# Optimization experiments

Measured on AMD Instinct MI355X. Metric: run time of the kernel, lower is better.

The kernel has to match this reference:

```python
import jax, jax.numpy as jnp
import numpy as np

K = 32          # init k
E = 0.003       # EMA rate e


def setup_inputs() -> dict:
    key = jax.random.key(0)
    k1, _ = jax.random.split(key)
    features = jax.random.normal(k1, (512, 6, 8192), dtype=jnp.float32)
    threshold = jnp.zeros((1,), dtype=jnp.float32)
    return {"features": features, "threshold": threshold}


def reference(features, threshold):
    batch_size, n_layers, d_features = features.shape
    batch_k = K * batch_size * n_layers
    flat = features.reshape(-1)                      # [B*L*D]
    topk_vals, topk_idxs = jax.lax.top_k(flat, batch_k)
    topk_vals = jax.nn.relu(topk_vals)
    out = jnp.zeros_like(flat).at[topk_idxs].set(topk_vals)
    out = out.reshape(batch_size, n_layers, d_features)
    min_k = jax.lax.stop_gradient(jnp.min(topk_vals))
    new_threshold = (1.0 - E) * threshold + E * min_k
    return out, new_threshold
```

## Files before the change

kernel.cpp:

```cpp
#include <hip/hip_runtime.h>
#include <stdint.h>

#define K_TOTAL   98304u
#define EMA_RATE  0.003f

#define SBINS      16384
#define SBIN_SHIFT 18
#define SAMPLE_VEC 131072
#define STARGET    8192u
#define P2_BINS    4096
#define P2_SHIFT   12
#define LCAP       1024
#define CAP2       65536u
#define EQCAP      256

#define MP_BLOCKS  3072
#define MP_UNROLL  8

__device__ __forceinline__ unsigned f2key(float x) {
    unsigned u = __float_as_uint(x);
    return (u & 0x80000000u) ? ~u : (u | 0x80000000u);
}
__device__ __forceinline__ float key2f(unsigned key) {
    unsigned u = (key & 0x80000000u) ? (key & 0x7FFFFFFFu) : ~key;
    return __uint_as_float(u);
}

__global__ __launch_bounds__(256) void sample_hist_kernel(
        const float4* __restrict__ in, unsigned* __restrict__ shist) {
    __shared__ unsigned h[SBINS];
    for (int i = threadIdx.x; i < SBINS; i += 256) h[i] = 0;
    __syncthreads();
    unsigned tid = blockIdx.x * 256 + threadIdx.x;
    unsigned nth = gridDim.x * 256;
    float4 v[4];
    #pragma unroll
    for (int u = 0; u < 4; ++u) {
        unsigned j = tid + u * nth;
        v[u] = (j < SAMPLE_VEC) ? in[j] : make_float4(0.f, 0.f, 0.f, 0.f);
    }
    #pragma unroll
    for (int u = 0; u < 4; ++u) {
        unsigned j = tid + u * nth;
        if (j < SAMPLE_VEC) {
            atomicAdd(&h[f2key(v[u].x) >> SBIN_SHIFT], 1u);
            atomicAdd(&h[f2key(v[u].y) >> SBIN_SHIFT], 1u);
            atomicAdd(&h[f2key(v[u].z) >> SBIN_SHIFT], 1u);
            atomicAdd(&h[f2key(v[u].w) >> SBIN_SHIFT], 1u);
        }
    }
    __syncthreads();
    for (int i = threadIdx.x; i < SBINS; i += 256) {
        unsigned c = h[i];
        if (c) atomicAdd(&shist[i], c);
    }
}

__global__ __launch_bounds__(1024) void sample_scan_kernel(
        const unsigned* __restrict__ shist, unsigned* __restrict__ res) {
    __shared__ unsigned psum[1024];
    const int T = 1024;
    const int GB = SBINS / T;
    int t = threadIdx.x;
    int hi = SBINS - 1 - t * GB;
    unsigned c[GB];
    #pragma unroll
    for (int j = 0; j < GB; ++j) c[j] = shist[hi - j];
    unsigned s = 0;
    #pragma unroll
    for (int j = 0; j < GB; ++j) s += c[j];
    psum[t] = s;
    __syncthreads();
    for (int off = 1; off < T; off <<= 1) {
        unsigned o = (t >= off) ? psum[t - off] : 0u;
        __syncthreads();
        psum[t] += o;
        __syncthreads();
    }
    unsigned cum = psum[t] - s;
    for (int j = 0; j < GB; ++j) {
        if (cum < STARGET && cum + c[j] >= STARGET) {
            unsigned bin = (unsigned)(hi - j);
            unsigned bb = (bin > 0) ? bin - 1 : 0;
            res[0] = bb << SBIN_SHIFT;
        }
        cum += c[j];
    }
}

__global__ __launch_bounds__(256) void main_pass_kernel(
        const float4* __restrict__ in, const unsigned* __restrict__ res,
        float* __restrict__ cval, unsigned* __restrict__ cidx,
        unsigned* __restrict__ gcnt, unsigned cap, int nvec) {
    __shared__ float    lval[LCAP];
    __shared__ unsigned lidx[LCAP];
    __shared__ unsigned lcnt, lbase;
    if (threadIdx.x == 0) lcnt = 0;
    __syncthreads();
    unsigned base = res[0];
    unsigned tid = blockIdx.x * 256 + threadIdx.x;
    unsigned nth = gridDim.x * 256;
    for (unsigned i0 = tid; i0 < (unsigned)nvec; i0 += MP_UNROLL * nth) {
        float4 v[MP_UNROLL];
        #pragma unroll
        for (int u = 0; u < MP_UNROLL; ++u) {
            unsigned j = i0 + u * nth;
            v[u] = (j < (unsigned)nvec) ? in[j]
                   : make_float4(-1e30f, -1e30f, -1e30f, -1e30f);
        }
        #pragma unroll
        for (int u = 0; u < MP_UNROLL; ++u) {
            unsigned j = i0 + u * nth;
            unsigned idx = 4u * j;
            float xs[4] = {v[u].x, v[u].y, v[u].z, v[u].w};
            #pragma unroll
            for (int c = 0; c < 4; ++c) {
                unsigned key = f2key(xs[c]);
                if (key >= base) {
                    unsigned p = atomicAdd(&lcnt, 1u);
                    if (p < LCAP) { lval[p] = xs[c]; lidx[p] = idx + c; }
                    else {
                        unsigned q = atomicAdd(gcnt, 1u);
                        if (q < cap) { cval[q] = xs[c]; cidx[q] = idx + c; }
                    }
                }
            }
        }
    }
    __syncthreads();
    unsigned n = min(lcnt, (unsigned)LCAP);
    if (threadIdx.x == 0) lbase = atomicAdd(gcnt, n);
    __syncthreads();
    for (unsigned j = threadIdx.x; j < n; j += 256) {
        unsigned p = lbase + j;
        if (p < cap) { cval[p] = lval[j]; cidx[p] = lidx[j]; }
    }
}

__global__ __launch_bounds__(256) void cand_hist_kernel(
        const float* __restrict__ cval, const unsigned* __restrict__ gcnt,
        const unsigned* __restrict__ res, unsigned* __restrict__ ghist,
        unsigned cap) {
    __shared__ unsigned h[P2_BINS];
    for (int i = threadIdx.x; i < P2_BINS; i += 256) h[i] = 0;
    __syncthreads();
    unsigned nc = min(*gcnt, cap);
    unsigned base = res[0];
    unsigned tid = blockIdx.x * 256 + threadIdx.x;
    unsigned nth = gridDim.x * 256;
    for (unsigned i0 = tid; i0 < nc; i0 += 4 * nth) {
        float v[4];
        #pragma unroll
        for (int u = 0; u < 4; ++u) {
            unsigned j = i0 + u * nth;
            v[u] = (j < nc) ? cval[j] : -1e30f;
        }
        #pragma unroll
        for (int u = 0; u < 4; ++u) {
            unsigned j = i0 + u * nth;
            if (j < nc) {
                unsigned g = (f2key(v[u]) - base) >> P2_SHIFT;
                if (g > P2_BINS - 1) g = P2_BINS - 1;
                atomicAdd(&h[g], 1u);
            }
        }
    }
    __syncthreads();
    for (int i = threadIdx.x; i < P2_BINS; i += 256) {
        unsigned c = h[i];
        if (c) atomicAdd(&ghist[i], c);
    }
}

__global__ __launch_bounds__(1024) void find_g_kernel(
        const unsigned* __restrict__ ghist, unsigned* __restrict__ res2) {
    __shared__ unsigned psum[1024];
    const int T = 1024;
    const int GB = P2_BINS / T;
    int t = threadIdx.x;
    int hi = P2_BINS - 1 - t * GB;
    unsigned c[GB];
    #pragma unroll
    for (int j = 0; j < GB; ++j) c[j] = ghist[hi - j];
    unsigned s = 0;
    #pragma unroll
    for (int j = 0; j < GB; ++j) s += c[j];
    psum[t] = s;
    __syncthreads();
    for (int off = 1; off < T; off <<= 1) {
        unsigned o = (t >= off) ? psum[t - off] : 0u;
        __syncthreads();
        psum[t] += o;
        __syncthreads();
    }
    unsigned cum = psum[t] - s;
    for (int j = 0; j < GB; ++j) {
        if (cum < K_TOTAL && cum + c[j] >= K_TOTAL) {
            res2[0] = (unsigned)(hi - j);
            res2[1] = K_TOTAL - cum;
        }
        cum += c[j];
    }
}

__global__ __launch_bounds__(256) void scatter_kernel(
        const float* __restrict__ cval, const unsigned* __restrict__ cidx,
        const unsigned* __restrict__ gcnt, const unsigned* __restrict__ res,
        const unsigned* __restrict__ res2,
        float* __restrict__ cval2, unsigned* __restrict__ cidx2,
        unsigned* __restrict__ cnt2, unsigned cap,
        float* __restrict__ out) {
    unsigned nc = min(*gcnt, cap);
    unsigned base = res[0];
    unsigned gstar = res2[0];
    unsigned tid = blockIdx.x * 256 + threadIdx.x;
    unsigned nth = gridDim.x * 256;
    for (unsigned i0 = tid; i0 < nc; i0 += 4 * nth) {
        float v[4];
        #pragma unroll
        for (int u = 0; u < 4; ++u) {
            unsigned j = i0 + u * nth;
            v[u] = (j < nc) ? cval[j] : -1e30f;
        }
        #pragma unroll
        for (int u = 0; u < 4; ++u) {
            unsigned j = i0 + u * nth;
            if (j < nc) {
                unsigned g = (f2key(v[u]) - base) >> P2_SHIFT;
                if (g > P2_BINS - 1) g = P2_BINS - 1;
                if (g > gstar) {
                    out[cidx[j]] = fmaxf(v[u], 0.0f);
                } else if (g == gstar) {
                    unsigned p = atomicAdd(cnt2, 1u);
                    if (p < CAP2) { cval2[p] = v[u]; cidx2[p] = cidx[j]; }
                }
            }
        }
    }
}

__global__ __launch_bounds__(256) void final_kernel(
        const float* __restrict__ cval2, const unsigned* __restrict__ cidx2,
        const unsigned* __restrict__ cnt2,
        const unsigned* __restrict__ res, const unsigned* __restrict__ res2,
        float* __restrict__ out,
        const float* __restrict__ thr_in, float* __restrict__ thr_out) {
    __shared__ unsigned h[1 << P2_SHIFT];
    __shared__ unsigned psum[256];
    __shared__ unsigned eqidx[EQCAP];
    __shared__ unsigned eqcnt;
    __shared__ unsigned sh_low, sh_need3;
    const int NB = 1 << P2_SHIFT;
    int t = threadIdx.x;
    unsigned nc2   = min(*cnt2, CAP2);
    unsigned base3 = res[0] + (res2[0] << P2_SHIFT);
    unsigned need2 = res2[1];

    for (int i = t; i < NB; i += 256) h[i] = 0;
    if (t == 0) eqcnt = 0;
    __syncthreads();
    for (unsigned i = t; i < nc2; i += 256) {
        unsigned low = f2key(cval2[i]) - base3;
        if (low > (unsigned)(NB - 1)) low = NB - 1;
        atomicAdd(&h[low], 1u);
    }
    __syncthreads();

    const int GB = NB / 256;
    int hi = NB - 1 - t * GB;
    unsigned s = 0;
    for (int j = 0; j < GB; ++j) s += h[hi - j];
    psum[t] = s;
    __syncthreads();
    for (int off = 1; off < 256; off <<= 1) {
        unsigned o = (t >= off) ? psum[t - off] : 0u;
        __syncthreads();
        psum[t] += o;
        __syncthreads();
    }
    unsigned cum = psum[t] - s;
    for (int j = 0; j < GB; ++j) {
        unsigned c = h[hi - j];
        if (cum < need2 && cum + c >= need2) {
            sh_low = (unsigned)(hi - j);
            sh_need3 = need2 - cum;
        }
        cum += c;
    }
    __syncthreads();
    unsigned kth_key = base3 + sh_low;
    unsigned need3   = sh_need3;

    for (unsigned i = t; i < nc2; i += 256) {
        float x = cval2[i];
        unsigned key = f2key(x);
        if (key > kth_key) {
            out[cidx2[i]] = fmaxf(x, 0.0f);
        } else if (key == kth_key) {
            unsigned p = atomicAdd(&eqcnt, 1u);
            if (p < EQCAP) eqidx[p] = cidx2[i];
        }
    }
    __syncthreads();

    unsigned ne = min(eqcnt, (unsigned)EQCAP);
    float vv = key2f(kth_key);
    for (unsigned e = t; e < ne; e += 256) {
        unsigned my = eqidx[e];
        unsigned rank = 0;
        for (unsigned f = 0; f < ne; ++f) rank += (eqidx[f] < my) ? 1u : 0u;
        if (rank < need3) out[my] = fmaxf(vv, 0.0f);
    }

    if (t == 0) {
        float mink = fmaxf(vv, 0.0f);
        thr_out[0] = (1.0f - EMA_RATE) * thr_in[0] + EMA_RATE * mink;
    }
}

extern "C" void kernel_launch(void* const* d_in, const int* in_sizes, int n_in,
                              void* d_out, int out_size, void* d_ws, size_t ws_size,
                              hipStream_t stream) {
    const float* feat   = (const float*)d_in[0];
    const float* thr_in = (const float*)d_in[1];
    float* out = (float*)d_out;
    int N    = in_sizes[0];
    int nvec = N / 4;

    uint8_t* w = (uint8_t*)d_ws;
    unsigned* shist = (unsigned*)w;
    unsigned* ghist = (unsigned*)(w + (64 << 10));
    unsigned* ctr   = (unsigned*)(w + (80 << 10));
    unsigned* gcnt  = ctr + 0;
    unsigned* cnt2  = ctr + 1;
    unsigned* res   = ctr + 4;
    unsigned* res2  = ctr + 8;

    size_t cand_off = (size_t)1 << 20;
    size_t avail    = (ws_size > cand_off + (CAP2 * 8 + 4096))
                        ? (ws_size - cand_off - CAP2 * 8 - 4096) / 8 : 0;
    unsigned cap = (unsigned)((avail < (size_t)(4u << 20)) ? avail : (size_t)(4u << 20));
    float*    cval  = (float*)(w + cand_off);
    unsigned* cidx  = (unsigned*)(w + cand_off + (size_t)cap * 4);
    float*    cval2 = (float*)(w + cand_off + (size_t)cap * 8);
    unsigned* cidx2 = (unsigned*)(w + cand_off + (size_t)cap * 8 + CAP2 * 4);

    hipMemsetAsync(d_ws, 0, (80 << 10) + 64, stream);
    hipMemsetAsync(d_out, 0, (size_t)N * 4, stream);

    sample_hist_kernel<<<128, 256, 0, stream>>>((const float4*)feat, shist);
    sample_scan_kernel<<<1,  1024, 0, stream>>>(shist, res);
    main_pass_kernel  <<<MP_BLOCKS, 256, 0, stream>>>((const float4*)feat, res,
                                                      cval, cidx, gcnt, cap, nvec);
    cand_hist_kernel  <<<128, 256, 0, stream>>>(cval, gcnt, res, ghist, cap);
    find_g_kernel     <<<1,  1024, 0, stream>>>(ghist, res2);
    scatter_kernel    <<<128, 256, 0, stream>>>(cval, cidx, gcnt, res, res2,
                                                cval2, cidx2, cnt2, cap, out);
    final_kernel      <<<1,   256, 0, stream>>>(cval2, cidx2, cnt2, res, res2,
                                                out, thr_in, out + N);
}
```

Baseline: 238.4 us.

## Fuse output zeroing into main pass and use per-wave ballot compaction buffers

The main pass now writes zeros to the output while streaming the input, so the separate output memset is no longer needed. Candidate compaction uses per-wave ballot and mbcnt prefix offsets into fixed per-wave regions instead of shared-memory atomics, with a global overflow buffer. Candidates are stored as (key, index) pairs, so later kernels skip the float-to-key conversion. In exchange, the histogram and scatter kernels must now scan every fixed-size wave slot, and the overflow capacity is bounded.

```diff
diff --git a/kernel.cpp b/kernel.cpp
--- a/kernel.cpp
+++ b/kernel.cpp
@@ -10,12 +10,14 @@
 #define STARGET    8192u
 #define P2_BINS    4096
 #define P2_SHIFT   12
-#define LCAP       1024
 #define CAP2       65536u
 #define EQCAP      256
 
-#define MP_BLOCKS  3072
-#define MP_UNROLL  8
+#define MP_BLOCKS  1024
+#define MP_THREADS 256
+#define NWAVES     4096
+#define WCAP       256
+#define OCAP       65536u
 
 __device__ __forceinline__ unsigned f2key(float x) {
     unsigned u = __float_as_uint(x);
@@ -33,21 +35,12 @@
     __syncthreads();
     unsigned tid = blockIdx.x * 256 + threadIdx.x;
     unsigned nth = gridDim.x * 256;
-    float4 v[4];
-    #pragma unroll
-    for (int u = 0; u < 4; ++u) {
-        unsigned j = tid + u * nth;
-        v[u] = (j < SAMPLE_VEC) ? in[j] : make_float4(0.f, 0.f, 0.f, 0.f);
-    }
-    #pragma unroll
-    for (int u = 0; u < 4; ++u) {
-        unsigned j = tid + u * nth;
-        if (j < SAMPLE_VEC) {
-            atomicAdd(&h[f2key(v[u].x) >> SBIN_SHIFT], 1u);
-            atomicAdd(&h[f2key(v[u].y) >> SBIN_SHIFT], 1u);
-            atomicAdd(&h[f2key(v[u].z) >> SBIN_SHIFT], 1u);
-            atomicAdd(&h[f2key(v[u].w) >> SBIN_SHIFT], 1u);
-        }
+    for (unsigned j = tid; j < SAMPLE_VEC; j += nth) {
+        float4 v = in[j];
+        atomicAdd(&h[f2key(v.x) >> SBIN_SHIFT], 1u);
+        atomicAdd(&h[f2key(v.y) >> SBIN_SHIFT], 1u);
+        atomicAdd(&h[f2key(v.z) >> SBIN_SHIFT], 1u);
+        atomicAdd(&h[f2key(v.w) >> SBIN_SHIFT], 1u);
     }
     __syncthreads();
     for (int i = threadIdx.x; i < SBINS; i += 256) {
@@ -88,82 +81,73 @@
     }
 }
 
-__global__ __launch_bounds__(256) void main_pass_kernel(
-        const float4* __restrict__ in, const unsigned* __restrict__ res,
-        float* __restrict__ cval, unsigned* __restrict__ cidx,
-        unsigned* __restrict__ gcnt, unsigned cap, int nvec) {
-    __shared__ float    lval[LCAP];
-    __shared__ unsigned lidx[LCAP];
-    __shared__ unsigned lcnt, lbase;
-    if (threadIdx.x == 0) lcnt = 0;
+__global__ __launch_bounds__(MP_THREADS) void main_pass_kernel(
+        const float4* __restrict__ in, float4* __restrict__ out,
+        const unsigned* __restrict__ res,
+        uint2* __restrict__ wreg, unsigned* __restrict__ wcnt,
+        uint2* __restrict__ ovf, unsigned* __restrict__ ocnt, int nvec) {
+    unsigned tid  = blockIdx.x * MP_THREADS + threadIdx.x;
+    unsigned nth  = gridDim.x * MP_THREADS;
+    unsigned gw   = tid >> 6;
+    unsigned lane = threadIdx.x & 63u;
+    unsigned base = res[0];
+    uint2* wb = wreg + (size_t)gw * WCAP;
+    unsigned wcount = 0;
+    const float4 z4 = make_float4(0.f, 0.f, 0.f, 0.f);
+    for (unsigned i = tid; i < (unsigned)nvec; i += nth) {
+        float4 v = in[i];
+        out[i] = z4;
+        unsigned idx = 4u * i;
+        float xs[4] = {v.x, v.y, v.z, v.w};
+        #pragma unroll
+        for (int c = 0; c < 4; ++c) {
+            unsigned key = f2key(xs[c]);
+            bool pred = key >= base;
+            unsigned long long mask = __ballot(pred);
+            if (mask) {
+                if (pred) {
+                    unsigned prefix = __builtin_amdgcn_mbcnt_hi(
+                        (unsigned)(mask >> 32),
+                        __builtin_amdgcn_mbcnt_lo((unsigned)mask, 0u));
+                    unsigned off = wcount + prefix;
+                    if (off < WCAP) {
+                        wb[off] = make_uint2(key, idx + c);
+                    } else {
+                        unsigned q = atomicAdd(ocnt, 1u);
+                        if (q < OCAP) ovf[q] = make_uint2(key, idx + c);
+                    }
+                }
+                wcount += (unsigned)__popcll(mask);
+            }
+        }
+    }
+    if (lane == 0) wcnt[gw] = (wcount < WCAP) ? wcount : WCAP;
+}
+
+__global__ __launch_bounds__(256) void cand_hist_kernel(
+        const uint2* __restrict__ wreg, const unsigned* __restrict__ wcnt,
+        const uint2* __restrict__ ovf, const unsigned* __restrict__ ocnt,
+        const unsigned* __restrict__ res, unsigned* __restrict__ ghist) {
+    __shared__ unsigned h[P2_BINS];
+    for (int i = threadIdx.x; i < P2_BINS; i += 256) h[i] = 0;
     __syncthreads();
     unsigned base = res[0];
     unsigned tid = blockIdx.x * 256 + threadIdx.x;
     unsigned nth = gridDim.x * 256;
-    for (unsigned i0 = tid; i0 < (unsigned)nvec; i0 += MP_UNROLL * nth) {
-        float4 v[MP_UNROLL];
-        #pragma unroll
-        for (int u = 0; u < MP_UNROLL; ++u) {
-            unsigned j = i0 + u * nth;
-            v[u] = (j < (unsigned)nvec) ? in[j]
-                   : make_float4(-1e30f, -1e30f, -1e30f, -1e30f);
-        }
-        #pragma unroll
-        for (int u = 0; u < MP_UNROLL; ++u) {
-            unsigned j = i0 + u * nth;
-            unsigned idx = 4u * j;
-            float xs[4] = {v[u].x, v[u].y, v[u].z, v[u].w};
-            #pragma unroll
-            for (int c = 0; c < 4; ++c) {
-                unsigned key = f2key(xs[c]);
-                if (key >= base) {
-                    unsigned p = atomicAdd(&lcnt, 1u);
-                    if (p < LCAP) { lval[p] = xs[c]; lidx[p] = idx + c; }
-                    else {
-                        unsigned q = atomicAdd(gcnt, 1u);
-                        if (q < cap) { cval[q] = xs[c]; cidx[q] = idx + c; }
-                    }
-                }
-            }
-        }
-    }
-    __syncthreads();
-    unsigned n = min(lcnt, (unsigned)LCAP);
-    if (threadIdx.x == 0) lbase = atomicAdd(gcnt, n);
-    __syncthreads();
-    for (unsigned j = threadIdx.x; j < n; j += 256) {
-        unsigned p = lbase + j;
-        if (p < cap) { cval[p] = lval[j]; cidx[p] = lidx[j]; }
-    }
-}
-
-__global__ __launch_bounds__(256) void cand_hist_kernel(
-        const float* __restrict__ cval, const unsigned* __restrict__ gcnt,
-        const unsigned* __restrict__ res, unsigned* __restrict__ ghist,
-        unsigned cap) {
-    __shared__ unsigned h[P2_BINS];
-    for (int i = threadIdx.x; i < P2_BINS; i += 256) h[i] = 0;
-    __syncthreads();
-    unsigned nc = min(*gcnt, cap);
-    unsigned base = res[0];
-    unsigned tid = blockIdx.x * 256 + threadIdx.x;
-    unsigned nth = gridDim.x * 256;
-    for (unsigned i0 = tid; i0 < nc; i0 += 4 * nth) {
-        float v[4];
-        #pragma unroll
-        for (int u = 0; u < 4; ++u) {
-            unsigned j = i0 + u * nth;
-            v[u] = (j < nc) ? cval[j] : -1e30f;
-        }
-        #pragma unroll
-        for (int u = 0; u < 4; ++u) {
-            unsigned j = i0 + u * nth;
-            if (j < nc) {
-                unsigned g = (f2key(v[u]) - base) >> P2_SHIFT;
-                if (g > P2_BINS - 1) g = P2_BINS - 1;
-                atomicAdd(&h[g], 1u);
-            }
-        }
+    const unsigned NSLOT = NWAVES * WCAP;
+    for (unsigned s = tid; s < NSLOT; s += nth) {
+        unsigned w = s >> 8, j = s & 255u;
+        if (j < wcnt[w]) {
+            unsigned g = (wreg[s].x - base) >> P2_SHIFT;
+            if (g > P2_BINS - 1) g = P2_BINS - 1;
+            atomicAdd(&h[g], 1u);
+        }
+    }
+    unsigned no = min(*ocnt, OCAP);
+    for (unsigned s = tid; s < no; s += nth) {
+        unsigned g = (ovf[s].x - base) >> P2_SHIFT;
+        if (g > P2_BINS - 1) g = P2_BINS - 1;
+        atomicAdd(&h[g], 1u);
     }
     __syncthreads();
     for (int i = threadIdx.x; i < P2_BINS; i += 256) {
@@ -204,43 +188,46 @@
 }
 
 __global__ __launch_bounds__(256) void scatter_kernel(
-        const float* __restrict__ cval, const unsigned* __restrict__ cidx,
-        const unsigned* __restrict__ gcnt, const unsigned* __restrict__ res,
-        const unsigned* __restrict__ res2,
-        float* __restrict__ cval2, unsigned* __restrict__ cidx2,
-        unsigned* __restrict__ cnt2, unsigned cap,
-        float* __restrict__ out) {
-    unsigned nc = min(*gcnt, cap);
-    unsigned base = res[0];
+        const uint2* __restrict__ wreg, const unsigned* __restrict__ wcnt,
+        const uint2* __restrict__ ovf, const unsigned* __restrict__ ocnt,
+        const unsigned* __restrict__ res, const unsigned* __restrict__ res2,
+        unsigned* __restrict__ kval2, unsigned* __restrict__ cidx2,
+        unsigned* __restrict__ cnt2, float* __restrict__ out) {
+    unsigned base  = res[0];
     unsigned gstar = res2[0];
     unsigned tid = blockIdx.x * 256 + threadIdx.x;
     unsigned nth = gridDim.x * 256;
-    for (unsigned i0 = tid; i0 < nc; i0 += 4 * nth) {
-        float v[4];
-        #pragma unroll
-        for (int u = 0; u < 4; ++u) {
-            unsigned j = i0 + u * nth;
-            v[u] = (j < nc) ? cval[j] : -1e30f;
-        }
-        #pragma unroll
-        for (int u = 0; u < 4; ++u) {
-            unsigned j = i0 + u * nth;
-            if (j < nc) {
-                unsigned g = (f2key(v[u]) - base) >> P2_SHIFT;
-                if (g > P2_BINS - 1) g = P2_BINS - 1;
-                if (g > gstar) {
-                    out[cidx[j]] = fmaxf(v[u], 0.0f);
-                } else if (g == gstar) {
-                    unsigned p = atomicAdd(cnt2, 1u);
-                    if (p < CAP2) { cval2[p] = v[u]; cidx2[p] = cidx[j]; }
-                }
+    const unsigned NSLOT = NWAVES * WCAP;
+    for (unsigned s = tid; s < NSLOT; s += nth) {
+        unsigned w = s >> 8, j = s & 255u;
+        if (j < wcnt[w]) {
+            uint2 e = wreg[s];
+            unsigned g = (e.x - base) >> P2_SHIFT;
+            if (g > P2_BINS - 1) g = P2_BINS - 1;
+            if (g > gstar) {
+                out[e.y] = fmaxf(key2f(e.x), 0.0f);
+            } else if (g == gstar) {
+                unsigned p = atomicAdd(cnt2, 1u);
+                if (p < CAP2) { kval2[p] = e.x; cidx2[p] = e.y; }
             }
         }
     }
+    unsigned no = min(*ocnt, OCAP);
+    for (unsigned s = tid; s < no; s += nth) {
+        uint2 e = ovf[s];
+        unsigned g = (e.x - base) >> P2_SHIFT;
+        if (g > P2_BINS - 1) g = P2_BINS - 1;
+        if (g > gstar) {
+            out[e.y] = fmaxf(key2f(e.x), 0.0f);
+        } else if (g == gstar) {
+            unsigned p = atomicAdd(cnt2, 1u);
+            if (p < CAP2) { kval2[p] = e.x; cidx2[p] = e.y; }
+        }
+    }
 }
 
 __global__ __launch_bounds__(256) void final_kernel(
-        const float* __restrict__ cval2, const unsigned* __restrict__ cidx2,
+        const unsigned* __restrict__ kval2, const unsigned* __restrict__ cidx2,
         const unsigned* __restrict__ cnt2,
         const unsigned* __restrict__ res, const unsigned* __restrict__ res2,
         float* __restrict__ out,
@@ -260,7 +247,7 @@
     if (t == 0) eqcnt = 0;
     __syncthreads();
     for (unsigned i = t; i < nc2; i += 256) {
-        unsigned low = f2key(cval2[i]) - base3;
+        unsigned low = kval2[i] - base3;
         if (low > (unsigned)(NB - 1)) low = NB - 1;
         atomicAdd(&h[low], 1u);
     }
@@ -292,10 +279,9 @@
     unsigned need3   = sh_need3;
 
     for (unsigned i = t; i < nc2; i += 256) {
-        float x = cval2[i];
-        unsigned key = f2key(x);
+        unsigned key = kval2[i];
         if (key > kth_key) {
-            out[cidx2[i]] = fmaxf(x, 0.0f);
+            out[cidx2[i]] = fmaxf(key2f(key), 0.0f);
         } else if (key == kth_key) {
             unsigned p = atomicAdd(&eqcnt, 1u);
             if (p < EQCAP) eqidx[p] = cidx2[i];
@@ -331,31 +317,27 @@
     unsigned* shist = (unsigned*)w;
     unsigned* ghist = (unsigned*)(w + (64 << 10));
     unsigned* ctr   = (unsigned*)(w + (80 << 10));
-    unsigned* gcnt  = ctr + 0;
+    unsigned* ocnt  = ctr + 0;
     unsigned* cnt2  = ctr + 1;
     unsigned* res   = ctr + 4;
     unsigned* res2  = ctr + 8;
-
-    size_t cand_off = (size_t)1 << 20;
-    size_t avail    = (ws_size > cand_off + (CAP2 * 8 + 4096))
-                        ? (ws_size - cand_off - CAP2 * 8 - 4096) / 8 : 0;
-    unsigned cap = (unsigned)((avail < (size_t)(4u << 20)) ? avail : (size_t)(4u << 20));
-    float*    cval  = (float*)(w + cand_off);
-    unsigned* cidx  = (unsigned*)(w + cand_off + (size_t)cap * 4);
-    float*    cval2 = (float*)(w + cand_off + (size_t)cap * 8);
-    unsigned* cidx2 = (unsigned*)(w + cand_off + (size_t)cap * 8 + CAP2 * 4);
-
-    hipMemsetAsync(d_ws, 0, (80 << 10) + 64, stream);
-    hipMemsetAsync(d_out, 0, (size_t)N * 4, stream);
+    unsigned* wcnt  = (unsigned*)(w + (84 << 10));
+
+    uint2*    wreg  = (uint2*)(w + ((size_t)1 << 20));
+    uint2*    ovf   = (uint2*)(w + ((size_t)9 << 20));
+    unsigned* kval2 = (unsigned*)(w + ((size_t)10 << 20));
+    unsigned* cidx2 = (unsigned*)(w + ((size_t)10 << 20) + CAP2 * 4);
+
+    hipMemsetAsync(d_ws, 0, (84 << 10), stream);
 
     sample_hist_kernel<<<128, 256, 0, stream>>>((const float4*)feat, shist);
     sample_scan_kernel<<<1,  1024, 0, stream>>>(shist, res);
-    main_pass_kernel  <<<MP_BLOCKS, 256, 0, stream>>>((const float4*)feat, res,
-                                                      cval, cidx, gcnt, cap, nvec);
-    cand_hist_kernel  <<<128, 256, 0, stream>>>(cval, gcnt, res, ghist, cap);
+    main_pass_kernel  <<<MP_BLOCKS, MP_THREADS, 0, stream>>>(
+        (const float4*)feat, (float4*)out, res, wreg, wcnt, ovf, ocnt, nvec);
+    cand_hist_kernel  <<<128, 256, 0, stream>>>(wreg, wcnt, ovf, ocnt, res, ghist);
     find_g_kernel     <<<1,  1024, 0, stream>>>(ghist, res2);
-    scatter_kernel    <<<128, 256, 0, stream>>>(cval, cidx, gcnt, res, res2,
-                                                cval2, cidx2, cnt2, cap, out);
-    final_kernel      <<<1,   256, 0, stream>>>(cval2, cidx2, cnt2, res, res2,
+    scatter_kernel    <<<128, 256, 0, stream>>>(wreg, wcnt, ovf, ocnt, res, res2,
+                                                kval2, cidx2, cnt2, out);
+    final_kernel      <<<1,   256, 0, stream>>>(kval2, cidx2, cnt2, res, res2,
                                                 out, thr_in, out + N);
 }
```

After: 242.4 us. About the same (+1.7%).
